# Kernel tuning notes

Measured on AMD Instinct MI355X. Metric: run time of the kernel, lower is better.

Reference implementation:

```python
import jax, jax.numpy as jnp
import numpy as np

H = 16      # q heads
G = 4       # groups (n_rep)
THETA = 10000.0


def _rope(x, cos, sin):
    # x pairs adjacent elements (torch complex view of reshape(..., -1, 2))
    x0 = x[..., ::2]
    x1 = x[..., 1::2]
    r0 = x0 * cos - x1 * sin
    r1 = x0 * sin + x1 * cos
    return jnp.stack([r0, r1], axis=-1).reshape(x.shape)


def setup_inputs() -> dict:
    key = jax.random.key(0)
    ks = jax.random.split(key, 5)
    B, S, D = 2, 2048, 1024
    return {
        "x": jax.random.normal(ks[0], (B, S, D), jnp.float32),
        "Wq": jax.random.normal(ks[1], (D, D), jnp.float32) * 0.02,
        "Wk": jax.random.normal(ks[2], (D, D // G), jnp.float32) * 0.02,
        "Wv": jax.random.normal(ks[3], (D, D // G), jnp.float32) * 0.02,
        "Wo": jax.random.normal(ks[4], (D, D), jnp.float32) * 0.02,
    }


def reference(x, Wq, Wk, Wv, Wo):
    B, S, D = x.shape
    hd = D // H                     # head dim = 64
    Hkv = H // G                    # kv heads = 4

    q = x @ Wq                      # (B,S,D)
    k = x @ Wk                      # (B,S,D/G)
    v = x @ Wv                      # (B,S,D/G)

    # repeat_kv: (B,S,Hkv,hd) -> (B,S,H,hd)
    k = jnp.repeat(k.reshape(B, S, Hkv, hd), G, axis=2)
    v = jnp.repeat(v.reshape(B, S, Hkv, hd), G, axis=2)

    # RoPE angles: freqs precomputed over hidden_dim (as in source)
    inv = 1.0 / (THETA ** (jnp.arange(0, D, 2, dtype=jnp.float32) / D))  # (D/2,)
    ang = jnp.arange(S, dtype=jnp.float32)[:, None] * inv[None, :]       # (S,D/2)
    q = _rope(q, jnp.cos(ang)[None], jnp.sin(ang)[None])                 # (B,S,D)
    angk = ang[:, : hd // 2]                                             # (S,hd/2)
    k = _rope(k, jnp.cos(angk)[None, :, None, :], jnp.sin(angk)[None, :, None, :])

    q = q.reshape(B, S, H, hd).transpose(0, 2, 1, 3)   # (B,H,S,hd)
    k = k.transpose(0, 2, 1, 3)
    v = v.transpose(0, 2, 1, 3)

    # NOTE: scale uses sqrt(hidden_dim), faithful to source
    scores = jnp.einsum('bhqd,bhkd->bhqk', q, k) / jnp.sqrt(jnp.float32(D))
    p = jax.nn.softmax(scores, axis=-1)
    o = jnp.einsum('bhqk,bhkd->bhqd', p, v)
    o = o.transpose(0, 2, 1, 3).reshape(B, S, D)
    return o @ Wo
```

## Files before the change

### kernel.cpp

```cpp
#include <hip/hip_runtime.h>
#include <math.h>

#define BATCH 2
#define SEQ   2048
#define DMODEL 1024
#define KDIM  1024
#define NH    16
#define HDIM  64
#define GRP   4
#define NKV   4
#define NSPLIT 4

enum { M_PLAIN = 0, M_QKV = 1 };

#define LN_THETA 9.210340371976184f

typedef short bf8_t __attribute__((ext_vector_type(8)));
typedef float f4_t __attribute__((ext_vector_type(4)));
typedef unsigned short us4_t __attribute__((ext_vector_type(4)));
typedef unsigned short us8_t __attribute__((ext_vector_type(8)));
typedef _Float16 h_t;
typedef _Float16 h4_t __attribute__((ext_vector_type(4)));

#define QB_OFF 0
#define KB_OFF 4194304
#define VB_OFF (4194304 + 1048576)

__device__ __forceinline__ unsigned short f2bf(float f) {
  unsigned int u = __float_as_uint(f);
  u += 0x7fffu + ((u >> 16) & 1u);
  return (unsigned short)(u >> 16);
}

__device__ __forceinline__ void gload_lds16(const void* g, void* l) {
  typedef __attribute__((address_space(1))) unsigned int gu32;
  typedef __attribute__((address_space(3))) unsigned int lu32;
  __builtin_amdgcn_global_load_lds((const gu32*)g, (lu32*)l, 16, 0, 0);
}

__global__ __launch_bounds__(256) void conv_x(const float* __restrict__ in,
                                              unsigned short* __restrict__ out) {
  const int i = blockIdx.x * 256 + threadIdx.x;
  float4 v = ((const float4*)in)[i];
  us4_t o = {f2bf(v.x), f2bf(v.y), f2bf(v.z), f2bf(v.w)};
  ((us4_t*)out)[i] = o;
}

__global__ __launch_bounds__(256) void convT_all(const float* __restrict__ W0,
                                                 const float* __restrict__ W1,
                                                 const float* __restrict__ W2,
                                                 const float* __restrict__ W3,
                                                 unsigned short* __restrict__ Wqkvt,
                                                 unsigned short* __restrict__ Wot) {
  const float* W; unsigned short* out; int N, rowoff;
  switch (blockIdx.z) {
    case 0: W = W0; out = Wqkvt; N = 1024; rowoff = 0;    break;
    case 1: W = W1; out = Wqkvt; N = 256;  rowoff = 1024; break;
    case 2: W = W2; out = Wqkvt; N = 256;  rowoff = 1280; break;
    default: W = W3; out = Wot;  N = 1024; rowoff = 0;    break;
  }
  const int n0 = blockIdx.x * 64;
  if (n0 >= N) return;
  __shared__ unsigned short T[64][72];
  const int t = threadIdx.x;
  const int k0 = blockIdx.y * 64;
  const int kr = t >> 4, n4 = (t & 15) * 4;
#pragma unroll
  for (int i = 0; i < 4; ++i) {
    const int k = kr + i * 16;
    float4 v = *(const float4*)&W[(size_t)(k0 + k) * N + n0 + n4];
    T[n4 + 0][k] = f2bf(v.x);
    T[n4 + 1][k] = f2bf(v.y);
    T[n4 + 2][k] = f2bf(v.z);
    T[n4 + 3][k] = f2bf(v.w);
  }
  __syncthreads();
#pragma unroll
  for (int i = 0; i < 2; ++i) {
    const int c = t + i * 256;
    const int n = c >> 3, kc = (c & 7) * 8;
    us8_t v = *(const us8_t*)&T[n][kc];
    *(us8_t*)&out[(size_t)(rowoff + n0 + n) * KDIM + k0 + kc] = v;
  }
}

template <int MODE>
__global__ __launch_bounds__(256, 3) void gemm_bf16(const unsigned short* __restrict__ A,
                                                    const unsigned short* __restrict__ Bt,
                                                    void* __restrict__ Cdst_, int N) {
  __shared__ __align__(16) unsigned short As[64 * 64];
  __shared__ __align__(16) unsigned short Bs[128 * 64];

  const int tid = threadIdx.x;
  const int lane = tid & 63, quad = lane >> 4, l16 = lane & 15;
  const int w = tid >> 6, wm = w >> 1, wn = w & 1;
  const int row0 = blockIdx.x * 64, col0 = blockIdx.y * 128;

  const int m0 = tid >> 2;
  const int kc0 = (tid & 3) ^ ((m0 >> 1) & 3);
  const unsigned short* Ag0 = A + (size_t)(row0 + m0) * KDIM + kc0 * 8;
  const unsigned short* Bg0 = Bt + (size_t)(col0 + m0) * KDIM + kc0 * 8;
  unsigned short* Al0 = &As[tid * 8];
  unsigned short* Bl0 = &Bs[tid * 8];

  int aoff[2][2], boff[4][2];
#pragma unroll
  for (int mi = 0; mi < 2; ++mi) {
    const int am = wm * 32 + mi * 16 + l16;
    const int sw = quad ^ ((am >> 1) & 3);
#pragma unroll
    for (int kh = 0; kh < 2; ++kh)
      aoff[mi][kh] = kh * 2048 + (((am << 2) | sw) << 3);
  }
#pragma unroll
  for (int ni = 0; ni < 4; ++ni) {
    const int bn = wn * 64 + ni * 16 + l16;
    const int sw = quad ^ ((bn >> 1) & 3);
#pragma unroll
    for (int kh = 0; kh < 2; ++kh)
      boff[ni][kh] = kh * 4096 + (((bn << 2) | sw) << 3);
  }

  f4_t acc[2][4];
#pragma unroll
  for (int mi = 0; mi < 2; ++mi)
#pragma unroll
    for (int ni = 0; ni < 4; ++ni) acc[mi][ni] = (f4_t){0.f, 0.f, 0.f, 0.f};

  for (int kb = 0; kb < KDIM; kb += 64) {
    __syncthreads();
    gload_lds16(Ag0 + kb,       Al0);
    gload_lds16(Ag0 + kb + 32,  Al0 + 2048);
    gload_lds16(Bg0 + kb,                     Bl0);
    gload_lds16(Bg0 + (size_t)64 * KDIM + kb, Bl0 + 2048);
    gload_lds16(Bg0 + kb + 32,                     Bl0 + 4096);
    gload_lds16(Bg0 + (size_t)64 * KDIM + kb + 32, Bl0 + 6144);
    __syncthreads();

    bf8_t af[2][2], bfr[4][2];
#pragma unroll
    for (int mi = 0; mi < 2; ++mi)
#pragma unroll
      for (int kh = 0; kh < 2; ++kh) af[mi][kh] = *(const bf8_t*)&As[aoff[mi][kh]];
#pragma unroll
    for (int ni = 0; ni < 4; ++ni)
#pragma unroll
      for (int kh = 0; kh < 2; ++kh) bfr[ni][kh] = *(const bf8_t*)&Bs[boff[ni][kh]];
#pragma unroll
    for (int kh = 0; kh < 2; ++kh)
#pragma unroll
      for (int mi = 0; mi < 2; ++mi)
#pragma unroll
        for (int ni = 0; ni < 4; ++ni)
          acc[mi][ni] = __builtin_amdgcn_mfma_f32_16x16x32_bf16(af[mi][kh], bfr[ni][kh], acc[mi][ni], 0, 0, 0);
  }

  if constexpr (MODE == M_PLAIN) {
    float* out = (float*)Cdst_;
#pragma unroll
    for (int mi = 0; mi < 2; ++mi) {
      const int rowb = row0 + wm * 32 + mi * 16 + quad * 4;
#pragma unroll
      for (int ni = 0; ni < 4; ++ni) {
        const int n = col0 + wn * 64 + ni * 16 + l16;
#pragma unroll
        for (int r = 0; r < 4; ++r)
          out[(size_t)(rowb + r) * N + n] = acc[mi][ni][r];
      }
    }
  } else {
    unsigned short* Qb = (unsigned short*)Cdst_;
    unsigned short* Kb = Qb + (KB_OFF - QB_OFF);
    unsigned short* Vb = Qb + (VB_OFF - QB_OFF);
#pragma unroll
    for (int ni = 0; ni < 4; ++ni) {
      const int nb = col0 + wn * 64 + ni * 16;
      const int n = nb + l16;
      if (nb < 1024) {
        const float inv = expf(-(float)(2 * (n >> 1)) * (LN_THETA / (float)DMODEL));
        const float sgn = (n & 1) ? 1.f : -1.f;
        const int h = n >> 6, d = n & 63;
#pragma unroll
        for (int mi = 0; mi < 2; ++mi) {
          const int rowb = row0 + wm * 32 + mi * 16 + quad * 4;
#pragma unroll
          for (int r = 0; r < 4; ++r) {
            const int row = rowb + r;
            const int bb = row >> 11, s = row & (SEQ - 1);
            const float v = acc[mi][ni][r];
            const float p = __shfl_xor(v, 1);
            float sn, cs;
            sincosf((float)s * inv, &sn, &cs);
            const float res = (v * cs + sgn * p * sn) * 0.03125f;
            Qb[((size_t)(bb * NH + h) * SEQ + s) * HDIM + d] = f2bf(res);
          }
        }
      } else if (nb < 1280) {
        const int nk = n - 1024;
        const int hkv = nk >> 6, d = nk & 63;
        const float inv = expf(-(float)(2 * (d >> 1)) * (LN_THETA / (float)DMODEL));
        const float sgn = (nk & 1) ? 1.f : -1.f;
#pragma unroll
        for (int mi = 0; mi < 2; ++mi) {
          const int rowb = row0 + wm * 32 + mi * 16 + quad * 4;
#pragma unroll
          for (int r = 0; r < 4; ++r) {
            const int row = rowb + r;
            const int bb = row >> 11, s = row & (SEQ - 1);
            const float v = acc[mi][ni][r];
            const float p = __shfl_xor(v, 1);
            float sn, cs;
            sincosf((float)s * inv, &sn, &cs);
            const float res = v * cs + sgn * p * sn;
            Kb[((size_t)(bb * NKV + hkv) * SEQ + s) * HDIM + d] = f2bf(res);
          }
        }
      } else {
        const int nv = n - 1280;
        const int hkv = nv >> 6, d = nv & 63;
#pragma unroll
        for (int mi = 0; mi < 2; ++mi) {
          const int s0 = row0 + wm * 32 + mi * 16 + quad * 4;
          const int bb = s0 >> 11, sl = s0 & (SEQ - 1);
          const int st = sl & 63;
          const int ps = (sl & ~63) | (st & 0x20) | ((st & 0x0C) << 1) | ((st & 0x10) >> 2);
          us4_t stv = {f2bf(acc[mi][ni][0]), f2bf(acc[mi][ni][1]),
                       f2bf(acc[mi][ni][2]), f2bf(acc[mi][ni][3])};
          *(us4_t*)&Vb[((size_t)(bb * NKV + hkv) * HDIM + d) * SEQ + ps] = stv;
        }
      }
    }
  }
}

__global__ __launch_bounds__(256, 4) void attn_fwd(const unsigned short* __restrict__ Q,
                                                   const unsigned short* __restrict__ K,
                                                   const unsigned short* __restrict__ V,
                                                   h_t* __restrict__ Opart,
                                                   float* __restrict__ Lpart) {
  __shared__ __align__(16) unsigned short Kt[4096];
  __shared__ __align__(16) unsigned short Vt[4096];

  const int b = blockIdx.x >> 4;
  const int h = blockIdx.x & (NH - 1);
  const int hkv = h >> 2;
  const int q0 = blockIdx.y * 128;
  const int sp = blockIdx.z;
  const int tid = threadIdx.x;
  const int w = tid >> 6;
  const int lane = tid & 63;
  const int quad = lane >> 4;
  const int l16 = lane & 15;

  const unsigned short* Qg = Q + ((size_t)(b * NH + h) * SEQ + q0 + w * 32) * HDIM;
  const unsigned short* Kg = K + (size_t)(b * NKV + hkv) * SEQ * HDIM;
  const unsigned short* Vg = V + (size_t)(b * NKV + hkv) * HDIM * SEQ;

  bf8_t qb[2][2];
#pragma unroll
  for (int g = 0; g < 2; ++g)
#pragma unroll
    for (int half = 0; half < 2; ++half)
      qb[g][half] = *(const bf8_t*)(Qg + (size_t)(g * 16 + l16) * HDIM + half * 32 + quad * 8);

  f4_t accO[2][4];
#pragma unroll
  for (int g = 0; g < 2; ++g)
#pragma unroll
    for (int d = 0; d < 4; ++d) accO[g][d] = (f4_t){0.f, 0.f, 0.f, 0.f};
  float accLs[2] = {0.f, 0.f};

  const int sw8 = (quad ^ ((l16 >> 1) & 3)) << 3;

  const int skey = tid >> 2;
  const int gc = ((tid & 3) ^ ((tid >> 3) & 3)) << 3;
  const unsigned short* KgA = Kg + (size_t)skey * HDIM + gc;
  const unsigned short* VgA = Vg + (size_t)skey * SEQ + gc;

  const int kbeg = sp * (SEQ / NSPLIT);
  const int kend = kbeg + SEQ / NSPLIT;
  for (int k0 = kbeg; k0 < kend; k0 += 64) {
    __syncthreads();
    gload_lds16(KgA + (size_t)k0 * HDIM,      &Kt[tid * 8]);
    gload_lds16(KgA + (size_t)k0 * HDIM + 32, &Kt[tid * 8 + 2048]);
    gload_lds16(VgA + k0,      &Vt[tid * 8]);
    gload_lds16(VgA + k0 + 32, &Vt[tid * 8 + 2048]);
    __syncthreads();

    union { bf8_t bf; unsigned int dw[4]; } pa[2][2];
#pragma unroll
    for (int cb = 0; cb < 4; ++cb) {
      const int koff = (cb * 16 + l16) * 32 + sw8;
      bf8_t kf0 = *(const bf8_t*)&Kt[koff];
      bf8_t kf1 = *(const bf8_t*)&Kt[koff + 2048];
#pragma unroll
      for (int g = 0; g < 2; ++g) {
        f4_t s = (f4_t){0.f, 0.f, 0.f, 0.f};
        s = __builtin_amdgcn_mfma_f32_16x16x32_bf16(kf0, qb[g][0], s, 0, 0, 0);
        s = __builtin_amdgcn_mfma_f32_16x16x32_bf16(kf1, qb[g][1], s, 0, 0, 0);
        const float p0 = __expf(s[0]), p1 = __expf(s[1]);
        const float p2 = __expf(s[2]), p3 = __expf(s[3]);
        accLs[g] += (p0 + p1) + (p2 + p3);
        pa[g][cb >> 1].dw[(cb & 1) * 2 + 0] =
            __builtin_amdgcn_perm(__float_as_uint(p1) + 0x8000u,
                                  __float_as_uint(p0) + 0x8000u, 0x07060302u);
        pa[g][cb >> 1].dw[(cb & 1) * 2 + 1] =
            __builtin_amdgcn_perm(__float_as_uint(p3) + 0x8000u,
                                  __float_as_uint(p2) + 0x8000u, 0x07060302u);
      }
    }

#pragma unroll
    for (int db = 0; db < 4; ++db) {
      const int voff = (db * 16 + l16) * 32 + sw8;
      bf8_t vf0 = *(const bf8_t*)&Vt[voff];
      bf8_t vf1 = *(const bf8_t*)&Vt[voff + 2048];
#pragma unroll
      for (int g = 0; g < 2; ++g) {
        accO[g][db] = __builtin_amdgcn_mfma_f32_16x16x32_bf16(pa[g][0].bf, vf0, accO[g][db], 0, 0, 0);
        accO[g][db] = __builtin_amdgcn_mfma_f32_16x16x32_bf16(pa[g][1].bf, vf1, accO[g][db], 0, 0, 0);
      }
    }
  }

#pragma unroll
  for (int g = 0; g < 2; ++g) {
    accLs[g] += __shfl_xor(accLs[g], 16);
    accLs[g] += __shfl_xor(accLs[g], 32);
  }

  h_t* Osp = Opart + (size_t)sp * BATCH * SEQ * NH * HDIM;
  float* Lsp = Lpart + (size_t)sp * BATCH * SEQ * NH;
#pragma unroll
  for (int g = 0; g < 2; ++g)
#pragma unroll
    for (int r = 0; r < 4; ++r) {
      const int q = q0 + w * 32 + g * 16 + quad * 4 + r;
      const size_t rowi = ((size_t)b * SEQ + q) * NH + h;
      h_t* op = Osp + rowi * HDIM;
#pragma unroll
      for (int db = 0; db < 4; ++db)
        op[db * 16 + l16] = (h_t)accO[g][db][r];
    }
  if (quad == 0) {
#pragma unroll
    for (int g = 0; g < 2; ++g) {
      const int q = q0 + w * 32 + g * 16 + l16;
      Lsp[((size_t)b * SEQ + q) * NH + h] = accLs[g];
    }
  }
}

__global__ __launch_bounds__(256) void attn_merge(const h_t* __restrict__ Opart,
                                                  const float* __restrict__ Lpart,
                                                  unsigned short* __restrict__ Ow) {
  const int idx = blockIdx.x * 256 + threadIdx.x;
  const int g = idx >> 4, j = (idx & 15) * 4;
  const size_t nq = (size_t)BATCH * SEQ * NH;
  float L = 0.f;
  float4 acc = make_float4(0.f, 0.f, 0.f, 0.f);
#pragma unroll
  for (int u = 0; u < NSPLIT; ++u) {
    L += Lpart[u * nq + g];
    h4_t o = *(const h4_t*)&Opart[((size_t)u * nq + g) * HDIM + j];
    acc.x += (float)o[0]; acc.y += (float)o[1];
    acc.z += (float)o[2]; acc.w += (float)o[3];
  }
  const float il = 1.0f / L;
  us4_t o = {f2bf(acc.x * il), f2bf(acc.y * il), f2bf(acc.z * il), f2bf(acc.w * il)};
  *(us4_t*)&Ow[(size_t)g * HDIM + j] = o;
}

extern "C" void kernel_launch(void* const* d_in, const int* in_sizes, int n_in,
                              void* d_out, int out_size, void* d_ws, size_t ws_size,
                              hipStream_t stream) {
  (void)in_sizes; (void)n_in; (void)out_size; (void)ws_size;
  const float* x  = (const float*)d_in[0];
  const float* Wq = (const float*)d_in[1];
  const float* Wk = (const float*)d_in[2];
  const float* Wv = (const float*)d_in[3];
  const float* Wo = (const float*)d_in[4];
  float* out = (float*)d_out;

  unsigned short* Qb    = (unsigned short*)d_ws;
  unsigned short* Kb    = Qb + 4194304;
  unsigned short* Vb    = Kb + 1048576;
  unsigned short* xb    = Vb + 1048576;
  unsigned short* Owb   = xb + 4194304;
  unsigned short* Wqkvt = Owb + 4194304;
  unsigned short* Wot   = Wqkvt + 1572864;
  h_t* Opart = (h_t*)(Wot + 1048576);
  float* Lpart = (float*)(Opart + (size_t)NSPLIT * 4194304);

  dim3 blk(256);
  conv_x<<<dim3(4096), blk, 0, stream>>>(x, xb);
  convT_all<<<dim3(16, 16, 4), blk, 0, stream>>>(Wq, Wk, Wv, Wo, Wqkvt, Wot);

  gemm_bf16<M_QKV><<<dim3(64, 12), blk, 0, stream>>>(xb, Wqkvt, Qb, 1536);
  attn_fwd<<<dim3(BATCH * NH, SEQ / 128, NSPLIT), blk, 0, stream>>>(Qb, Kb, Vb, Opart, Lpart);
  attn_merge<<<dim3(4096), blk, 0, stream>>>(Opart, Lpart, Owb);
  gemm_bf16<M_PLAIN><<<dim3(64, 8), blk, 0, stream>>>(Owb, Wot, out, DMODEL);
}
```

Measured before the change: 175.7 us.

## Double-buffer LDS in GEMM and attention, use exp2 softmax and halve key splits

Both the GEMM and attention main loops now double-buffer their LDS tiles. The next K-step's global-to-LDS loads are issued before computing on the current buffer, so only one barrier per iteration remains. Attention folds log2(e) into the Q scale so it can use the hardware exp2, and packs probabilities with v_cvt_pk_bf16_f32 instead of perm-based truncation. NSPLIT drops from 4 to 2, giving fewer partial outputs to combine but fewer attention blocks. LDS use doubles, which may reduce occupancy.

```diff
diff --git a/kernel.cpp b/kernel.cpp
--- a/kernel.cpp
+++ b/kernel.cpp
@@ -9,11 +9,12 @@
 #define HDIM  64
 #define GRP   4
 #define NKV   4
-#define NSPLIT 4
+#define NSPLIT 2
 
 enum { M_PLAIN = 0, M_QKV = 1 };
 
 #define LN_THETA 9.210340371976184f
+#define QSCALE 0.04508422002778f
 
 typedef short bf8_t __attribute__((ext_vector_type(8)));
 typedef float f4_t __attribute__((ext_vector_type(4)));
@@ -30,6 +31,14 @@
   unsigned int u = __float_as_uint(f);
   u += 0x7fffu + ((u >> 16) & 1u);
   return (unsigned short)(u >> 16);
+}
+
+__device__ __forceinline__ float fexp2(float x) {
+#if __has_builtin(__builtin_amdgcn_exp2f)
+  return __builtin_amdgcn_exp2f(x);
+#else
+  return exp2f(x);
+#endif
 }
 
 __device__ __forceinline__ void gload_lds16(const void* g, void* l) {
@@ -88,8 +97,8 @@
 __global__ __launch_bounds__(256, 3) void gemm_bf16(const unsigned short* __restrict__ A,
                                                     const unsigned short* __restrict__ Bt,
                                                     void* __restrict__ Cdst_, int N) {
-  __shared__ __align__(16) unsigned short As[64 * 64];
-  __shared__ __align__(16) unsigned short Bs[128 * 64];
+  __shared__ __align__(16) unsigned short As[2 * 64 * 64];
+  __shared__ __align__(16) unsigned short Bs[2 * 128 * 64];
 
   const int tid = threadIdx.x;
   const int lane = tid & 63, quad = lane >> 4, l16 = lane & 15;
@@ -103,6 +112,16 @@
   unsigned short* Al0 = &As[tid * 8];
   unsigned short* Bl0 = &Bs[tid * 8];
 
+#define STAGE_GEMM(c, kk)                                                      \
+  do {                                                                         \
+    gload_lds16(Ag0 + (kk),      Al0 + (c) * 4096);                            \
+    gload_lds16(Ag0 + (kk) + 32, Al0 + (c) * 4096 + 2048);                     \
+    gload_lds16(Bg0 + (kk),                          Bl0 + (c) * 8192);        \
+    gload_lds16(Bg0 + (size_t)64 * KDIM + (kk),      Bl0 + (c) * 8192 + 2048); \
+    gload_lds16(Bg0 + (kk) + 32,                     Bl0 + (c) * 8192 + 4096); \
+    gload_lds16(Bg0 + (size_t)64 * KDIM + (kk) + 32, Bl0 + (c) * 8192 + 6144); \
+  } while (0)
+
   int aoff[2][2], boff[4][2];
 #pragma unroll
   for (int mi = 0; mi < 2; ++mi) {
@@ -127,25 +146,23 @@
 #pragma unroll
     for (int ni = 0; ni < 4; ++ni) acc[mi][ni] = (f4_t){0.f, 0.f, 0.f, 0.f};
 
+  STAGE_GEMM(0, 0);
+  __syncthreads();
+  int cur = 0;
   for (int kb = 0; kb < KDIM; kb += 64) {
-    __syncthreads();
-    gload_lds16(Ag0 + kb,       Al0);
-    gload_lds16(Ag0 + kb + 32,  Al0 + 2048);
-    gload_lds16(Bg0 + kb,                     Bl0);
-    gload_lds16(Bg0 + (size_t)64 * KDIM + kb, Bl0 + 2048);
-    gload_lds16(Bg0 + kb + 32,                     Bl0 + 4096);
-    gload_lds16(Bg0 + (size_t)64 * KDIM + kb + 32, Bl0 + 6144);
-    __syncthreads();
-
+    if (kb + 64 < KDIM) STAGE_GEMM(cur ^ 1, kb + 64);
+
+    const unsigned short* Asc = As + cur * 4096;
+    const unsigned short* Bsc = Bs + cur * 8192;
     bf8_t af[2][2], bfr[4][2];
 #pragma unroll
     for (int mi = 0; mi < 2; ++mi)
 #pragma unroll
-      for (int kh = 0; kh < 2; ++kh) af[mi][kh] = *(const bf8_t*)&As[aoff[mi][kh]];
+      for (int kh = 0; kh < 2; ++kh) af[mi][kh] = *(const bf8_t*)&Asc[aoff[mi][kh]];
 #pragma unroll
     for (int ni = 0; ni < 4; ++ni)
 #pragma unroll
-      for (int kh = 0; kh < 2; ++kh) bfr[ni][kh] = *(const bf8_t*)&Bs[boff[ni][kh]];
+      for (int kh = 0; kh < 2; ++kh) bfr[ni][kh] = *(const bf8_t*)&Bsc[boff[ni][kh]];
 #pragma unroll
     for (int kh = 0; kh < 2; ++kh)
 #pragma unroll
@@ -153,7 +170,11 @@
 #pragma unroll
         for (int ni = 0; ni < 4; ++ni)
           acc[mi][ni] = __builtin_amdgcn_mfma_f32_16x16x32_bf16(af[mi][kh], bfr[ni][kh], acc[mi][ni], 0, 0, 0);
-  }
+
+    __syncthreads();
+    cur ^= 1;
+  }
+#undef STAGE_GEMM
 
   if constexpr (MODE == M_PLAIN) {
     float* out = (float*)Cdst_;
@@ -191,7 +212,7 @@
             const float p = __shfl_xor(v, 1);
             float sn, cs;
             sincosf((float)s * inv, &sn, &cs);
-            const float res = (v * cs + sgn * p * sn) * 0.03125f;
+            const float res = (v * cs + sgn * p * sn) * QSCALE;
             Qb[((size_t)(bb * NH + h) * SEQ + s) * HDIM + d] = f2bf(res);
           }
         }
@@ -238,8 +259,8 @@
                                                    const unsigned short* __restrict__ V,
                                                    h_t* __restrict__ Opart,
                                                    float* __restrict__ Lpart) {
-  __shared__ __align__(16) unsigned short Kt[4096];
-  __shared__ __align__(16) unsigned short Vt[4096];
+  __shared__ __align__(16) unsigned short Kt[2 * 4096];
+  __shared__ __align__(16) unsigned short Vt[2 * 4096];
 
   const int b = blockIdx.x >> 4;
   const int h = blockIdx.x & (NH - 1);
@@ -277,51 +298,64 @@
   const unsigned short* KgA = Kg + (size_t)skey * HDIM + gc;
   const unsigned short* VgA = Vg + (size_t)skey * SEQ + gc;
 
+#define STAGE_ATTN(c, kk)                                                          \
+  do {                                                                             \
+    gload_lds16(KgA + (size_t)(kk) * HDIM,      &Kt[(c) * 4096 + tid * 8]);        \
+    gload_lds16(KgA + (size_t)(kk) * HDIM + 32, &Kt[(c) * 4096 + tid * 8 + 2048]); \
+    gload_lds16(VgA + (kk),      &Vt[(c) * 4096 + tid * 8]);                       \
+    gload_lds16(VgA + (kk) + 32, &Vt[(c) * 4096 + tid * 8 + 2048]);                \
+  } while (0)
+
   const int kbeg = sp * (SEQ / NSPLIT);
   const int kend = kbeg + SEQ / NSPLIT;
+
+  STAGE_ATTN(0, kbeg);
+  __syncthreads();
+  int cur = 0;
   for (int k0 = kbeg; k0 < kend; k0 += 64) {
-    __syncthreads();
-    gload_lds16(KgA + (size_t)k0 * HDIM,      &Kt[tid * 8]);
-    gload_lds16(KgA + (size_t)k0 * HDIM + 32, &Kt[tid * 8 + 2048]);
-    gload_lds16(VgA + k0,      &Vt[tid * 8]);
-    gload_lds16(VgA + k0 + 32, &Vt[tid * 8 + 2048]);
-    __syncthreads();
+    if (k0 + 64 < kend) STAGE_ATTN(cur ^ 1, k0 + 64);
+
+    const unsigned short* Ktc = Kt + cur * 4096;
+    const unsigned short* Vtc = Vt + cur * 4096;
 
     union { bf8_t bf; unsigned int dw[4]; } pa[2][2];
 #pragma unroll
     for (int cb = 0; cb < 4; ++cb) {
       const int koff = (cb * 16 + l16) * 32 + sw8;
-      bf8_t kf0 = *(const bf8_t*)&Kt[koff];
-      bf8_t kf1 = *(const bf8_t*)&Kt[koff + 2048];
+      bf8_t kf0 = *(const bf8_t*)&Ktc[koff];
+      bf8_t kf1 = *(const bf8_t*)&Ktc[koff + 2048];
 #pragma unroll
       for (int g = 0; g < 2; ++g) {
         f4_t s = (f4_t){0.f, 0.f, 0.f, 0.f};
         s = __builtin_amdgcn_mfma_f32_16x16x32_bf16(kf0, qb[g][0], s, 0, 0, 0);
         s = __builtin_amdgcn_mfma_f32_16x16x32_bf16(kf1, qb[g][1], s, 0, 0, 0);
-        const float p0 = __expf(s[0]), p1 = __expf(s[1]);
-        const float p2 = __expf(s[2]), p3 = __expf(s[3]);
+        const float p0 = fexp2(s[0]), p1 = fexp2(s[1]);
+        const float p2 = fexp2(s[2]), p3 = fexp2(s[3]);
         accLs[g] += (p0 + p1) + (p2 + p3);
-        pa[g][cb >> 1].dw[(cb & 1) * 2 + 0] =
-            __builtin_amdgcn_perm(__float_as_uint(p1) + 0x8000u,
-                                  __float_as_uint(p0) + 0x8000u, 0x07060302u);
-        pa[g][cb >> 1].dw[(cb & 1) * 2 + 1] =
-            __builtin_amdgcn_perm(__float_as_uint(p3) + 0x8000u,
-                                  __float_as_uint(p2) + 0x8000u, 0x07060302u);
+        unsigned int w0, w1;
+        asm("v_cvt_pk_bf16_f32 %0, %1, %2" : "=v"(w0) : "v"(p0), "v"(p1));
+        asm("v_cvt_pk_bf16_f32 %0, %1, %2" : "=v"(w1) : "v"(p2), "v"(p3));
+        pa[g][cb >> 1].dw[(cb & 1) * 2 + 0] = w0;
+        pa[g][cb >> 1].dw[(cb & 1) * 2 + 1] = w1;
       }
     }
 
 #pragma unroll
     for (int db = 0; db < 4; ++db) {
       const int voff = (db * 16 + l16) * 32 + sw8;
-      bf8_t vf0 = *(const bf8_t*)&Vt[voff];
-      bf8_t vf1 = *(const bf8_t*)&Vt[voff + 2048];
+      bf8_t vf0 = *(const bf8_t*)&Vtc[voff];
+      bf8_t vf1 = *(const bf8_t*)&Vtc[voff + 2048];
 #pragma unroll
       for (int g = 0; g < 2; ++g) {
         accO[g][db] = __builtin_amdgcn_mfma_f32_16x16x32_bf16(pa[g][0].bf, vf0, accO[g][db], 0, 0, 0);
         accO[g][db] = __builtin_amdgcn_mfma_f32_16x16x32_bf16(pa[g][1].bf, vf1, accO[g][db], 0, 0, 0);
       }
     }
-  }
+
+    __syncthreads();
+    cur ^= 1;
+  }
+#undef STAGE_ATTN
 
 #pragma unroll
   for (int g = 0; g < 2; ++g) {
```

Measured after the change: 171.3 us. -2.5%, faster.
